# Kernel tuning notes

Hardware: AMD Instinct MI355X
Metric: run time of the kernel (lower is better)

## Reference

```python
import jax, jax.numpy as jnp
import numpy as np

VOXEL = 0.1  # voxel size used in NSLoss.voxelize


def _chamfer(x, y):
    """Squared-distance chamfer terms. x: [B,N,3], y: [B,M,3].
    Returns (dist1 [B,N]: min over y for each x point, dist2 [B,M])."""
    xx = jnp.sum(x * x, axis=-1)              # [B,N]
    yy = jnp.sum(y * y, axis=-1)              # [B,M]
    zz = jnp.einsum('bnd,bmd->bnm', x, y)     # [B,N,M]
    P = xx[:, :, None] + yy[None if False else slice(None), None, :][0] if False else xx[:, :, None] + yy[:, None, :] - 2.0 * zz
    return P.min(axis=2), P.min(axis=1)


def _voxelize(coord):
    # masked_fill(nan -> inf), per-batch min over points, quantize, truncate to int
    c = jnp.where(jnp.isnan(coord), jnp.inf, coord)
    gmin = c.min(axis=1, keepdims=True)       # [B,1,3]
    grid = ((coord - gmin) / VOXEL).astype(jnp.int32)  # trunc like torch .int()
    return jax.lax.stop_gradient(grid)        # torch .int() detaches grad


def setup_inputs() -> dict:
    key = jax.random.key(0)
    k1, k2 = jax.random.split(key)
    preds = jax.random.normal(k1, (2, 8192, 3), dtype=jnp.float32)
    gts = jax.random.normal(k2, (2, 8192, 3), dtype=jnp.float32)
    return {"preds": preds, "gts": gts}


def reference(preds, gts):
    # chamfer on raw coordinates
    d1, d2 = _chamfer(preds, gts)
    loss2 = d1.mean() + d2.mean()
    # chamfer on voxelized coordinates
    pv = _voxelize(preds).astype(jnp.float32)
    gv = _voxelize(gts).astype(jnp.float32)
    d1v, d2v = _chamfer(pv, gv)
    loss1 = d1v.mean() + d2v.mean()
    return loss1 + loss2
```

## Files before the change

### kernel.cpp

```cpp
#include <hip/hip_runtime.h>
#include <math.h>

#define B 2
#define N 8192
#define PTS_STRIDE (N*3)
#define VOXEL 0.1f

#define CBLK 128
#define PBLK 1024

#define WS_ACC 16
#define WS_TICKET 17
#define WS_GMIN 20
#define WS_MINS 32
#define MINS_TOTAL 65536
#define OFF_PACK (WS_MINS + MINS_TOTAL)
#define PERG 147456
#define OFF_AFLO(g) (OFF_PACK + (g)*PERG)
#define OFF_AFHI(g) (OFF_AFLO(g) + 32768)
#define OFF_BR(g)   (OFF_AFLO(g) + 65536)
#define OFF_BV(g)   (OFF_AFLO(g) + 98304)
#define OFF_XXR(g)  (OFF_AFLO(g) + 131072)
#define OFF_XXV(g)  (OFF_AFLO(g) + 139264)

typedef __attribute__((ext_vector_type(8))) short short8;
typedef __attribute__((ext_vector_type(16))) float f16v;

union S8 { short8 v; unsigned short u[8]; };

__device__ __forceinline__ unsigned short f2bf(float f) {
    unsigned u = __float_as_uint(f);
    return (unsigned short)((u + 0x7FFFu + ((u >> 16) & 1u)) >> 16);
}
__device__ __forceinline__ float bf2f(unsigned short h) {
    return __uint_as_float(((unsigned)h) << 16);
}
__device__ __forceinline__ float voxq(float v, float g) {
    return (float)(int)((v - g) / VOXEL);
}
__device__ __forceinline__ unsigned fenc(float f) {
    const unsigned u = __float_as_uint(f);
    return (u & 0x80000000u) ? ~u : (u | 0x80000000u);
}
__device__ __forceinline__ float fdec(unsigned k) {
    const unsigned u = (k & 0x80000000u) ? (k & 0x7FFFFFFFu) : ~k;
    return __uint_as_float(u);
}

__global__ void __launch_bounds__(PBLK)
gmin_kernel(const float* __restrict__ preds,
            const float* __restrict__ gts,
            float* __restrict__ ws) {
    const int g   = blockIdx.x;
    const int arr = g >> 1;
    const int b   = g & 1;
    const float4* base4 = (const float4*)((arr ? gts : preds) + b * PTS_STRIDE);

    float m0 = INFINITY, m1 = INFINITY, m2 = INFINITY;
#pragma unroll
    for (int j = 0; j < 2; ++j) {
        const int i = j * PBLK + threadIdx.x;
        const float4 q0 = base4[i*3+0];
        const float4 q1 = base4[i*3+1];
        const float4 q2 = base4[i*3+2];
        float v;
        v = q0.x; m0 = fminf(m0, (v!=v)?INFINITY:v);
        v = q0.w; m0 = fminf(m0, (v!=v)?INFINITY:v);
        v = q1.z; m0 = fminf(m0, (v!=v)?INFINITY:v);
        v = q2.y; m0 = fminf(m0, (v!=v)?INFINITY:v);
        v = q0.y; m1 = fminf(m1, (v!=v)?INFINITY:v);
        v = q1.x; m1 = fminf(m1, (v!=v)?INFINITY:v);
        v = q1.w; m1 = fminf(m1, (v!=v)?INFINITY:v);
        v = q2.z; m1 = fminf(m1, (v!=v)?INFINITY:v);
        v = q0.z; m2 = fminf(m2, (v!=v)?INFINITY:v);
        v = q1.y; m2 = fminf(m2, (v!=v)?INFINITY:v);
        v = q2.x; m2 = fminf(m2, (v!=v)?INFINITY:v);
        v = q2.w; m2 = fminf(m2, (v!=v)?INFINITY:v);
    }
    for (int off = 32; off; off >>= 1) {
        m0 = fminf(m0, __shfl_down(m0, off));
        m1 = fminf(m1, __shfl_down(m1, off));
        m2 = fminf(m2, __shfl_down(m2, off));
    }
    __shared__ float sm[16][3];
    const int wave = threadIdx.x >> 6, lane = threadIdx.x & 63;
    if (lane == 0) { sm[wave][0] = m0; sm[wave][1] = m1; sm[wave][2] = m2; }
    __syncthreads();
    if (threadIdx.x == 0) {
        float a0 = sm[0][0], a1 = sm[0][1], a2 = sm[0][2];
        for (int w = 1; w < 16; ++w) {
            a0 = fminf(a0, sm[w][0]);
            a1 = fminf(a1, sm[w][1]);
            a2 = fminf(a2, sm[w][2]);
        }
        ws[WS_GMIN + g*3+0] = a0; ws[WS_GMIN + g*3+1] = a1; ws[WS_GMIN + g*3+2] = a2;
        if (g == 0) { ws[WS_ACC] = 0.0f; ((unsigned*)ws)[WS_TICKET] = 0u; }
    }
}

__global__ void __launch_bounds__(256)
pack_kernel(const float* __restrict__ preds,
            const float* __restrict__ gts,
            float* __restrict__ ws) {
    const int i   = blockIdx.x * 256 + threadIdx.x;
    const int g   = i >> 13;
    const int idx = i & (N-1);
    const int arr = g >> 1;
    const int b   = g & 1;
    const float* base = (arr ? gts : preds) + b * PTS_STRIDE;

    unsigned* mins = (unsigned*)ws + WS_MINS;
    mins[i] = 0xFF800000u;
    mins[i + 32768] = 0xFF800000u;

    const float g0 = ws[WS_GMIN + g*3+0];
    const float g1 = ws[WS_GMIN + g*3+1];
    const float g2 = ws[WS_GMIN + g*3+2];

    const float p0 = base[idx*3+0], p1 = base[idx*3+1], p2 = base[idx*3+2];
    const float w0 = voxq(p0, g0), w1 = voxq(p1, g1), w2 = voxq(p2, g2);
    const float rr = fmaf(p0,p0, fmaf(p1,p1, p2*p2));
    const float vv = fmaf(w0,w0, fmaf(w1,w1, w2*w2));

    const unsigned short yyh = f2bf(rr);
    const unsigned short yyl = f2bf(rr - bf2f(yyh));
    const unsigned short vvh = f2bf(vv);
    const unsigned short vvl = f2bf(vv - bf2f(vvh));
    const unsigned short ONE = 0x3F80;

    short8* AFLO = (short8*)(ws + OFF_AFLO(g));
    short8* AFHI = (short8*)(ws + OFF_AFHI(g));
    short8* BR   = (short8*)(ws + OFF_BR(g));
    short8* BV   = (short8*)(ws + OFF_BV(g));

    S8 f;
    f.u[0]=f2bf(p0); f.u[1]=f2bf(p1); f.u[2]=f2bf(p2);
    f.u[3]=yyh; f.u[4]=yyl; f.u[5]=f2bf(w0); f.u[6]=f2bf(w1); f.u[7]=f2bf(w2);
    AFLO[idx] = f.v;
    f.u[0]=vvh; f.u[1]=vvl; f.u[2]=0; f.u[3]=0; f.u[4]=0; f.u[5]=0; f.u[6]=0; f.u[7]=0;
    AFHI[idx] = f.v;
    f.u[0]=f2bf(-2.0f*p0); f.u[1]=f2bf(-2.0f*p1); f.u[2]=f2bf(-2.0f*p2);
    f.u[3]=ONE; f.u[4]=ONE; f.u[5]=0; f.u[6]=0; f.u[7]=0;
    BR[idx] = f.v;
    f.u[0]=0; f.u[1]=0; f.u[2]=0; f.u[3]=0; f.u[4]=0;
    f.u[5]=f2bf(-2.0f*w0); f.u[6]=f2bf(-2.0f*w1); f.u[7]=f2bf(-2.0f*w2);
    BV[idx] = f.v;
    ws[OFF_XXR(g) + idx] = rr;
    ws[OFF_XXV(g) + idx] = vv;
}

__global__ void __launch_bounds__(CBLK, 6)
chamfer_kernel(float* __restrict__ ws) {
    const int tid  = threadIdx.x;
    const int wave = tid >> 6, lane = tid & 63;
    const int half = lane >> 5, c32 = lane & 31;
    const int slot = blockIdx.z;
    const int dir  = slot & 1;
    const int b    = slot >> 1;
    const int gX = dir*2 + b;
    const int gY = (1-dir)*2 + b;

    const short8* Abase = (const short8*)(ws + (half ? OFF_AFHI(gY) : OFF_AFLO(gY)));
    const short8* BR = (const short8*)(ws + OFF_BR(gX));
    const short8* BV = (const short8*)(ws + OFF_BV(gX));

    const int xbase = blockIdx.x * 32;
    S8 hc;
    hc.u[0] = (c32 < 16) ? (unsigned short)0 : (unsigned short)0x3F80;
    hc.u[1] = hc.u[0];
    hc.u[2]=0; hc.u[3]=0; hc.u[4]=0; hc.u[5]=0; hc.u[6]=0; hc.u[7]=0;
    const int xcol0 = xbase + (c32 & 15);
    const short8 bf0 = (half == 0) ? ((c32 < 16) ? BR[xcol0] : BV[xcol0]) : hc.v;
    const short8 bf1 = (half == 0) ? ((c32 < 16) ? BR[xcol0+16] : BV[xcol0+16]) : hc.v;

    float mn0 = INFINITY, mn1 = INFINITY;
    const f16v Z = (f16v)(0.0f);
    const int abase0 = (blockIdx.y * 2 + wave) * 1024 + c32;

#pragma unroll 2
    for (int t = 0; t < 32; ++t) {
        const short8 a = Abase[abase0 + t*32];
        const f16v d0 = __builtin_amdgcn_mfma_f32_32x32x16_bf16(a, bf0, Z, 0, 0, 0);
        {
            float t0 = fminf(fminf(d0[0], d0[1]),  fminf(d0[2], d0[3]));
            float t1 = fminf(fminf(d0[4], d0[5]),  fminf(d0[6], d0[7]));
            float t2 = fminf(fminf(d0[8], d0[9]),  fminf(d0[10], d0[11]));
            float t3 = fminf(fminf(d0[12], d0[13]), fminf(d0[14], d0[15]));
            mn0 = fminf(mn0, fminf(fminf(t0, t1), fminf(t2, t3)));
        }
        const f16v d1 = __builtin_amdgcn_mfma_f32_32x32x16_bf16(a, bf1, Z, 0, 0, 0);
        {
            float t0 = fminf(fminf(d1[0], d1[1]),  fminf(d1[2], d1[3]));
            float t1 = fminf(fminf(d1[4], d1[5]),  fminf(d1[6], d1[7]));
            float t2 = fminf(fminf(d1[8], d1[9]),  fminf(d1[10], d1[11]));
            float t3 = fminf(fminf(d1[12], d1[13]), fminf(d1[14], d1[15]));
            mn1 = fminf(mn1, fminf(fminf(t0, t1), fminf(t2, t3)));
        }
    }

    mn0 = fminf(mn0, __shfl_xor(mn0, 32));
    mn1 = fminf(mn1, __shfl_xor(mn1, 32));

    if (half == 0) {
        unsigned* mins = (unsigned*)ws + WS_MINS;
        const int var = (c32 < 16) ? 0 : 1;
        const int e0 = ((slot*2 + var) << 13) + xcol0;
        atomicMin(&mins[e0],      fenc(mn0));
        atomicMin(&mins[e0 + 16], fenc(mn1));
    }
}

__global__ void __launch_bounds__(256)
finalize_kernel(float* __restrict__ ws, float* __restrict__ out) {
    const int g = blockIdx.x * 256 + threadIdx.x;
    const int slot = g >> 13;
    const int x    = g & (N-1);
    const int dir  = slot & 1;
    const int b    = slot >> 1;
    const int gX   = dir*2 + b;
    const unsigned* mins = (const unsigned*)ws + WS_MINS;
    float s = fdec(mins[((slot*2 + 0) << 13) + x]) + ws[OFF_XXR(gX) + x]
            + fdec(mins[((slot*2 + 1) << 13) + x]) + ws[OFF_XXV(gX) + x];
    for (int off = 32; off; off >>= 1)
        s += __shfl_down(s, off);
    __shared__ float sm[4];
    const int wave = threadIdx.x >> 6, lane = threadIdx.x & 63;
    if (lane == 0) sm[wave] = s;
    __syncthreads();
    if (threadIdx.x == 0) {
        const float bs = sm[0] + sm[1] + sm[2] + sm[3];
        atomicAdd(ws + WS_ACC, bs);
        __threadfence();
        const unsigned t = atomicAdd(&((unsigned*)ws)[WS_TICKET], 1u);
        if (t == gridDim.x - 1) {
            __threadfence();
            const float total = atomicAdd(ws + WS_ACC, 0.0f);
            out[0] = total * (1.0f / 16384.0f);
        }
    }
}

extern "C" void kernel_launch(void* const* d_in, const int* in_sizes, int n_in,
                              void* d_out, int out_size, void* d_ws, size_t ws_size,
                              hipStream_t stream) {
    const float* preds = (const float*)d_in[0];
    const float* gts   = (const float*)d_in[1];
    float* ws  = (float*)d_ws;
    float* out = (float*)d_out;

    gmin_kernel<<<dim3(4), dim3(PBLK), 0, stream>>>(preds, gts, ws);
    pack_kernel<<<dim3(128), dim3(256), 0, stream>>>(preds, gts, ws);
    chamfer_kernel<<<dim3(N/32, 4, 4), dim3(CBLK), 0, stream>>>(ws);
    finalize_kernel<<<dim3(128), dim3(256), 0, stream>>>(ws, out);
}
```

Measured before the change: 91.71 us.

## Widen chamfer tiles to 64 columns and parallelize gmin across more blocks

The chamfer kernel now handles 64 x-columns per block with four MFMA tiles per A-fragment load instead of two. This reuses each loaded A fragment across twice as many columns and halves the grid size. The gmin reduction is split across 64 blocks of 256 threads writing partial minima, which pack_kernel then folds, so the serial 4-block reduction goes away. The min fold now uses three-operand min patterns, and the occupancy hint drops from 6 to 4, which trades register headroom for fewer waves.

```diff
diff --git a/kernel.cpp b/kernel.cpp
--- a/kernel.cpp
+++ b/kernel.cpp
@@ -7,11 +7,10 @@
 #define VOXEL 0.1f
 
 #define CBLK 128
-#define PBLK 1024
+#define XPB 64
 
 #define WS_ACC 16
 #define WS_TICKET 17
-#define WS_GMIN 20
 #define WS_MINS 32
 #define MINS_TOTAL 65536
 #define OFF_PACK (WS_MINS + MINS_TOTAL)
@@ -22,6 +21,7 @@
 #define OFF_BV(g)   (OFF_AFLO(g) + 98304)
 #define OFF_XXR(g)  (OFF_AFLO(g) + 131072)
 #define OFF_XXV(g)  (OFF_AFLO(g) + 139264)
+#define WS_PART (OFF_PACK + 4*PERG)
 
 typedef __attribute__((ext_vector_type(8))) short short8;
 typedef __attribute__((ext_vector_type(16))) float f16v;
@@ -46,55 +46,57 @@
     const unsigned u = (k & 0x80000000u) ? (k & 0x7FFFFFFFu) : ~k;
     return __uint_as_float(u);
 }
-
-__global__ void __launch_bounds__(PBLK)
+__device__ __forceinline__ float min3f(float a, float b, float c) {
+    return fminf(fminf(a, b), c);
+}
+__device__ __forceinline__ void fold16(const f16v d, float& mn) {
+    const float t0 = min3f(d[0],  d[1],  d[2]);
+    const float t1 = min3f(d[3],  d[4],  d[5]);
+    const float t2 = min3f(d[6],  d[7],  d[8]);
+    const float t3 = min3f(d[9],  d[10], d[11]);
+    const float t4 = min3f(d[12], d[13], d[14]);
+    const float u0 = min3f(t0, t1, t2);
+    const float u1 = min3f(t3, t4, d[15]);
+    mn = min3f(mn, u0, u1);
+}
+
+__global__ void __launch_bounds__(256)
 gmin_kernel(const float* __restrict__ preds,
             const float* __restrict__ gts,
             float* __restrict__ ws) {
-    const int g   = blockIdx.x;
+    const int blk = blockIdx.x;
+    const int g   = blk >> 4;
+    const int sub = blk & 15;
     const int arr = g >> 1;
     const int b   = g & 1;
-    const float4* base4 = (const float4*)((arr ? gts : preds) + b * PTS_STRIDE);
+    const float* base = (arr ? gts : preds) + b * PTS_STRIDE;
 
     float m0 = INFINITY, m1 = INFINITY, m2 = INFINITY;
 #pragma unroll
     for (int j = 0; j < 2; ++j) {
-        const int i = j * PBLK + threadIdx.x;
-        const float4 q0 = base4[i*3+0];
-        const float4 q1 = base4[i*3+1];
-        const float4 q2 = base4[i*3+2];
+        const int idx = (sub << 9) + (j << 8) + threadIdx.x;
         float v;
-        v = q0.x; m0 = fminf(m0, (v!=v)?INFINITY:v);
-        v = q0.w; m0 = fminf(m0, (v!=v)?INFINITY:v);
-        v = q1.z; m0 = fminf(m0, (v!=v)?INFINITY:v);
-        v = q2.y; m0 = fminf(m0, (v!=v)?INFINITY:v);
-        v = q0.y; m1 = fminf(m1, (v!=v)?INFINITY:v);
-        v = q1.x; m1 = fminf(m1, (v!=v)?INFINITY:v);
-        v = q1.w; m1 = fminf(m1, (v!=v)?INFINITY:v);
-        v = q2.z; m1 = fminf(m1, (v!=v)?INFINITY:v);
-        v = q0.z; m2 = fminf(m2, (v!=v)?INFINITY:v);
-        v = q1.y; m2 = fminf(m2, (v!=v)?INFINITY:v);
-        v = q2.x; m2 = fminf(m2, (v!=v)?INFINITY:v);
-        v = q2.w; m2 = fminf(m2, (v!=v)?INFINITY:v);
+        v = base[idx*3+0]; m0 = fminf(m0, (v!=v)?INFINITY:v);
+        v = base[idx*3+1]; m1 = fminf(m1, (v!=v)?INFINITY:v);
+        v = base[idx*3+2]; m2 = fminf(m2, (v!=v)?INFINITY:v);
     }
     for (int off = 32; off; off >>= 1) {
         m0 = fminf(m0, __shfl_down(m0, off));
         m1 = fminf(m1, __shfl_down(m1, off));
         m2 = fminf(m2, __shfl_down(m2, off));
     }
-    __shared__ float sm[16][3];
+    __shared__ float sm[4][3];
     const int wave = threadIdx.x >> 6, lane = threadIdx.x & 63;
     if (lane == 0) { sm[wave][0] = m0; sm[wave][1] = m1; sm[wave][2] = m2; }
     __syncthreads();
     if (threadIdx.x == 0) {
-        float a0 = sm[0][0], a1 = sm[0][1], a2 = sm[0][2];
-        for (int w = 1; w < 16; ++w) {
-            a0 = fminf(a0, sm[w][0]);
-            a1 = fminf(a1, sm[w][1]);
-            a2 = fminf(a2, sm[w][2]);
-        }
-        ws[WS_GMIN + g*3+0] = a0; ws[WS_GMIN + g*3+1] = a1; ws[WS_GMIN + g*3+2] = a2;
-        if (g == 0) { ws[WS_ACC] = 0.0f; ((unsigned*)ws)[WS_TICKET] = 0u; }
+        const float a0 = fminf(fminf(sm[0][0], sm[1][0]), fminf(sm[2][0], sm[3][0]));
+        const float a1 = fminf(fminf(sm[0][1], sm[1][1]), fminf(sm[2][1], sm[3][1]));
+        const float a2 = fminf(fminf(sm[0][2], sm[1][2]), fminf(sm[2][2], sm[3][2]));
+        ws[WS_PART + blk*3+0] = a0;
+        ws[WS_PART + blk*3+1] = a1;
+        ws[WS_PART + blk*3+2] = a2;
+        if (blk == 0) { ws[WS_ACC] = 0.0f; ((unsigned*)ws)[WS_TICKET] = 0u; }
     }
 }
 
@@ -113,9 +115,13 @@
     mins[i] = 0xFF800000u;
     mins[i + 32768] = 0xFF800000u;
 
-    const float g0 = ws[WS_GMIN + g*3+0];
-    const float g1 = ws[WS_GMIN + g*3+1];
-    const float g2 = ws[WS_GMIN + g*3+2];
+    float g0 = INFINITY, g1 = INFINITY, g2 = INFINITY;
+#pragma unroll
+    for (int w = 0; w < 16; ++w) {
+        g0 = fminf(g0, ws[WS_PART + (g*16 + w)*3 + 0]);
+        g1 = fminf(g1, ws[WS_PART + (g*16 + w)*3 + 1]);
+        g2 = fminf(g2, ws[WS_PART + (g*16 + w)*3 + 2]);
+    }
 
     const float p0 = base[idx*3+0], p1 = base[idx*3+1], p2 = base[idx*3+2];
     const float w0 = voxq(p0, g0), w1 = voxq(p1, g1), w2 = voxq(p2, g2);
@@ -149,7 +155,7 @@
     ws[OFF_XXV(g) + idx] = vv;
 }
 
-__global__ void __launch_bounds__(CBLK, 6)
+__global__ void __launch_bounds__(CBLK, 4)
 chamfer_kernel(float* __restrict__ ws) {
     const int tid  = threadIdx.x;
     const int wave = tid >> 6, lane = tid & 63;
@@ -164,42 +170,40 @@
     const short8* BR = (const short8*)(ws + OFF_BR(gX));
     const short8* BV = (const short8*)(ws + OFF_BV(gX));
 
-    const int xbase = blockIdx.x * 32;
+    const int xbase = blockIdx.x * XPB;
     S8 hc;
     hc.u[0] = (c32 < 16) ? (unsigned short)0 : (unsigned short)0x3F80;
     hc.u[1] = hc.u[0];
     hc.u[2]=0; hc.u[3]=0; hc.u[4]=0; hc.u[5]=0; hc.u[6]=0; hc.u[7]=0;
     const int xcol0 = xbase + (c32 & 15);
-    const short8 bf0 = (half == 0) ? ((c32 < 16) ? BR[xcol0] : BV[xcol0]) : hc.v;
-    const short8 bf1 = (half == 0) ? ((c32 < 16) ? BR[xcol0+16] : BV[xcol0+16]) : hc.v;
-
-    float mn0 = INFINITY, mn1 = INFINITY;
+    const short8* Bsel = (c32 < 16) ? BR : BV;
+    const short8 bf0 = (half == 0) ? Bsel[xcol0]      : hc.v;
+    const short8 bf1 = (half == 0) ? Bsel[xcol0 + 16] : hc.v;
+    const short8 bf2 = (half == 0) ? Bsel[xcol0 + 32] : hc.v;
+    const short8 bf3 = (half == 0) ? Bsel[xcol0 + 48] : hc.v;
+
+    float mn0 = INFINITY, mn1 = INFINITY, mn2 = INFINITY, mn3 = INFINITY;
     const f16v Z = (f16v)(0.0f);
     const int abase0 = (blockIdx.y * 2 + wave) * 1024 + c32;
 
 #pragma unroll 2
     for (int t = 0; t < 32; ++t) {
         const short8 a = Abase[abase0 + t*32];
-        const f16v d0 = __builtin_amdgcn_mfma_f32_32x32x16_bf16(a, bf0, Z, 0, 0, 0);
-        {
-            float t0 = fminf(fminf(d0[0], d0[1]),  fminf(d0[2], d0[3]));
-            float t1 = fminf(fminf(d0[4], d0[5]),  fminf(d0[6], d0[7]));
-            float t2 = fminf(fminf(d0[8], d0[9]),  fminf(d0[10], d0[11]));
-            float t3 = fminf(fminf(d0[12], d0[13]), fminf(d0[14], d0[15]));
-            mn0 = fminf(mn0, fminf(fminf(t0, t1), fminf(t2, t3)));
-        }
-        const f16v d1 = __builtin_amdgcn_mfma_f32_32x32x16_bf16(a, bf1, Z, 0, 0, 0);
-        {
-            float t0 = fminf(fminf(d1[0], d1[1]),  fminf(d1[2], d1[3]));
-            float t1 = fminf(fminf(d1[4], d1[5]),  fminf(d1[6], d1[7]));
-            float t2 = fminf(fminf(d1[8], d1[9]),  fminf(d1[10], d1[11]));
-            float t3 = fminf(fminf(d1[12], d1[13]), fminf(d1[14], d1[15]));
-            mn1 = fminf(mn1, fminf(fminf(t0, t1), fminf(t2, t3)));
-        }
+        f16v d;
+        d = __builtin_amdgcn_mfma_f32_32x32x16_bf16(a, bf0, Z, 0, 0, 0);
+        fold16(d, mn0);
+        d = __builtin_amdgcn_mfma_f32_32x32x16_bf16(a, bf1, Z, 0, 0, 0);
+        fold16(d, mn1);
+        d = __builtin_amdgcn_mfma_f32_32x32x16_bf16(a, bf2, Z, 0, 0, 0);
+        fold16(d, mn2);
+        d = __builtin_amdgcn_mfma_f32_32x32x16_bf16(a, bf3, Z, 0, 0, 0);
+        fold16(d, mn3);
     }
 
     mn0 = fminf(mn0, __shfl_xor(mn0, 32));
     mn1 = fminf(mn1, __shfl_xor(mn1, 32));
+    mn2 = fminf(mn2, __shfl_xor(mn2, 32));
+    mn3 = fminf(mn3, __shfl_xor(mn3, 32));
 
     if (half == 0) {
         unsigned* mins = (unsigned*)ws + WS_MINS;
@@ -207,6 +211,8 @@
         const int e0 = ((slot*2 + var) << 13) + xcol0;
         atomicMin(&mins[e0],      fenc(mn0));
         atomicMin(&mins[e0 + 16], fenc(mn1));
+        atomicMin(&mins[e0 + 32], fenc(mn2));
+        atomicMin(&mins[e0 + 48], fenc(mn3));
     }
 }
 
@@ -248,8 +254,8 @@
     float* ws  = (float*)d_ws;
     float* out = (float*)d_out;
 
-    gmin_kernel<<<dim3(4), dim3(PBLK), 0, stream>>>(preds, gts, ws);
+    gmin_kernel<<<dim3(64), dim3(256), 0, stream>>>(preds, gts, ws);
     pack_kernel<<<dim3(128), dim3(256), 0, stream>>>(preds, gts, ws);
-    chamfer_kernel<<<dim3(N/32, 4, 4), dim3(CBLK), 0, stream>>>(ws);
+    chamfer_kernel<<<dim3(N/XPB, 4, 4), dim3(CBLK), 0, stream>>>(ws);
     finalize_kernel<<<dim3(128), dim3(256), 0, stream>>>(ws, out);
 }
```

Measured after the change: 82.22 us. -10.3%, faster.
